# Optimization experiments

Hardware: AMD Instinct MI355X
Metric: run time of the kernel (lower is better)

## Reference

```python
import jax, jax.numpy as jnp
import numpy as np


def setup_inputs() -> dict:
    key = jax.random.key(0)
    ks = jax.random.split(key, 7)
    B, L, D, N = 4, 4096, 1024, 64
    x = jax.random.normal(ks[0], (B, L, D), dtype=jnp.float32)
    # nn.Linear weights: (out_features, in_features)
    W_in = jax.random.normal(ks[1], (N, D), dtype=jnp.float32) * (1.0 / np.sqrt(D))
    W_out = jax.random.normal(ks[2], (D, N), dtype=jnp.float32) * (1.0 / np.sqrt(N))
    log_A = jax.random.normal(ks[3], (N,), dtype=jnp.float32) * 0.02
    B_param = jax.random.normal(ks[4], (N,), dtype=jnp.float32) * 0.02
    C_param = jax.random.normal(ks[5], (N,), dtype=jnp.float32) * 0.02
    log_dt = jnp.float32(np.log(1.0))  # dt_init = 1.0
    return {"x": x, "W_in": W_in, "W_out": W_out, "log_A": log_A,
            "B_param": B_param, "C_param": C_param, "log_dt": log_dt}


def _zoh_discretize(log_A, B_param, log_dt):
    dt = jnp.exp(log_dt)
    A = -jnp.exp(log_A)
    Abar = jnp.exp(A * dt)
    eps = 1e-06
    small = jnp.abs(A) < eps
    denom = jnp.where(small, jnp.ones_like(A), A)
    frac = (Abar - 1.0) / denom
    frac = jnp.where(small, dt, frac)
    Bbar = frac * B_param
    return Abar, Bbar


def reference(x, W_in, W_out, log_A, B_param, C_param, log_dt):
    # x: (B, L, D)
    Bsz, L, D = x.shape
    N = log_A.shape[0]
    Abar, Bbar = _zoh_discretize(log_A, B_param, log_dt)
    u = jnp.einsum('bld,nd->bln', x, W_in)  # (B, L, N)

    def step(h, u_t):
        h = h * Abar + u_t * Bbar  # (B, N)
        return h, h * C_param

    h0 = jnp.zeros((Bsz, N), dtype=x.dtype)
    _, ys = jax.lax.scan(step, h0, jnp.swapaxes(u, 0, 1))  # ys: (L, B, N)
    y = jnp.swapaxes(ys, 0, 1)  # (B, L, N)
    return jnp.einsum('bln,dn->bld', y, W_out)  # (B, L, D)
```

## Files before the change

### kernel.cpp

```cpp
#include <hip/hip_runtime.h>
#include <math.h>

namespace {

constexpr int kB = 4;
constexpr int kL = 4096;
constexpr int kD = 1024;
constexpr int kN = 64;
constexpr int kM = kB * kL;
constexpr size_t kBLN = (size_t)kM * kN;
constexpr int kSplit = 8;
constexpr int kKRange = kD / kSplit;
constexpr int kBK1 = 32;
constexpr int kBK2 = 16;
constexpr int kChunks = 64;
constexpr int kChunkLen = kL / kChunks;
constexpr size_t kHloc = (size_t)kB * kChunks * kN;

template <bool kAtomic>
__global__ __launch_bounds__(64) void k_gemm_in(const float* __restrict__ x,
                                                const float* __restrict__ Win,
                                                float* __restrict__ u) {
  __shared__ __align__(16) float As[kBK1][68];
  __shared__ __align__(16) float Bs[kBK1][68];
  const int t = threadIdx.x;
  const int m_blk = blockIdx.x * 64;
  const int z = blockIdx.y;

  const int tm = t & 7;
  const int tn = t >> 3;
  const int m0 = tm * 8;
  const int n0 = tn * 8;

  const int kk = t & 31;
  const int half = t >> 5;

  float acc[8][8];
#pragma unroll
  for (int i = 0; i < 8; ++i)
#pragma unroll
    for (int j = 0; j < 8; ++j) acc[i][j] = 0.0f;

  for (int kc = 0; kc < kKRange; kc += kBK1) {
    const int k0 = z * kKRange + kc;
#pragma unroll
    for (int i = 0; i < 8; ++i) {
      const int m4 = half * 32 + i * 4;
      const float* src = &x[(size_t)(m_blk + m4) * kD + k0 + kk];
      float4 v = make_float4(src[0], src[kD], src[2 * kD], src[3 * kD]);
      *reinterpret_cast<float4*>(&As[kk][m4]) = v;
    }
#pragma unroll
    for (int i = 0; i < 8; ++i) {
      const int n4 = half * 32 + i * 4;
      const float* src = &Win[(size_t)n4 * kD + k0 + kk];
      float4 v = make_float4(src[0], src[kD], src[2 * kD], src[3 * kD]);
      *reinterpret_cast<float4*>(&Bs[kk][n4]) = v;
    }
    __syncthreads();

#pragma unroll 4
    for (int k = 0; k < kBK1; ++k) {
      float4 a0 = *reinterpret_cast<const float4*>(&As[k][m0]);
      float4 a1 = *reinterpret_cast<const float4*>(&As[k][m0 + 4]);
      float4 b0 = *reinterpret_cast<const float4*>(&Bs[k][n0]);
      float4 b1 = *reinterpret_cast<const float4*>(&Bs[k][n0 + 4]);
      float a[8] = {a0.x, a0.y, a0.z, a0.w, a1.x, a1.y, a1.z, a1.w};
      float b[8] = {b0.x, b0.y, b0.z, b0.w, b1.x, b1.y, b1.z, b1.w};
#pragma unroll
      for (int i = 0; i < 8; ++i)
#pragma unroll
        for (int j = 0; j < 8; ++j) acc[i][j] = fmaf(a[i], b[j], acc[i][j]);
    }
    __syncthreads();
  }

  if constexpr (kAtomic) {
#pragma unroll
    for (int i = 0; i < 8; ++i) {
      float* dst = &u[(size_t)(m_blk + m0 + i) * kN + n0];
#pragma unroll
      for (int j = 0; j < 8; ++j) atomicAdd(dst + j, acc[i][j]);
    }
  } else {
    float* up = u + (size_t)z * kBLN;
#pragma unroll
    for (int i = 0; i < 8; ++i) {
      const size_t o = (size_t)(m_blk + m0 + i) * kN + n0;
      *reinterpret_cast<float4*>(&up[o]) =
          make_float4(acc[i][0], acc[i][1], acc[i][2], acc[i][3]);
      *reinterpret_cast<float4*>(&up[o + 4]) =
          make_float4(acc[i][4], acc[i][5], acc[i][6], acc[i][7]);
    }
  }
}

__device__ __forceinline__ void zoh(const float* __restrict__ logA,
                                    const float* __restrict__ logdt, int n,
                                    float& A, float& dt, float& Abar) {
  dt = expf(logdt[0]);
  A = -expf(logA[n]);
  Abar = expf(A * dt);
}

__device__ __forceinline__ float zoh_bbar(float A, float dt, float Abar,
                                          float Bp) {
  const bool small = fabsf(A) < 1e-6f;
  const float denom = small ? 1.0f : A;
  float frac = (Abar - 1.0f) / denom;
  frac = small ? dt : frac;
  return frac * Bp;
}

template <int kParts>
__global__ __launch_bounds__(64) void k_scan_local(
    const float* __restrict__ logA, const float* __restrict__ Bparam,
    const float* __restrict__ logdt, float* __restrict__ u,
    float* __restrict__ hloc) {
  const int n = threadIdx.x;
  const int c = blockIdx.x;
  const int b = blockIdx.y;
  float A, dt, Abar;
  zoh(logA, logdt, n, A, dt, Abar);
  const float Bbar = zoh_bbar(A, dt, Abar, Bparam[n]);

  const size_t base = ((size_t)b * kL + (size_t)c * kChunkLen) * kN + n;

  float h = 0.0f;
#pragma unroll 8
  for (int s = 0; s < kChunkLen; ++s) {
    const size_t idx = base + (size_t)s * kN;
    float uu = 0.0f;
#pragma unroll
    for (int p = 0; p < kParts; ++p) uu += u[idx + (size_t)p * kBLN];
    const float ub = uu * Bbar;
    h = fmaf(h, Abar, ub);
    u[idx] = ub;
  }
  hloc[((size_t)b * kChunks + c) * kN + n] = h;
}

__global__ __launch_bounds__(64) void k_scan_apply(
    const float* __restrict__ logA, const float* __restrict__ Cparam,
    const float* __restrict__ logdt, const float* __restrict__ u,
    float* __restrict__ ybuf, const float* __restrict__ hloc) {
  const int n = threadIdx.x;
  const int c = blockIdx.x;
  const int b = blockIdx.y;
  float A, dt, Abar;
  zoh(logA, logdt, n, A, dt, Abar);
  const float C = Cparam[n];
  const float AbarC = expf(A * dt * (float)kChunkLen);

  const size_t hbase = (size_t)b * kChunks * kN + n;

  float h = 0.0f;
  if (c > 0) {
    float p0 = hloc[hbase];
    float p1 = (c > 1) ? hloc[hbase + kN] : 0.0f;
    for (int j = 0; j < c; ++j) {
      const float cur = p0;
      p0 = p1;
      p1 = (j + 2 < c) ? hloc[hbase + (size_t)(j + 2) * kN] : 0.0f;
      h = fmaf(h, AbarC, cur);
    }
  }

  const size_t base = ((size_t)b * kL + (size_t)c * kChunkLen) * kN + n;
#pragma unroll 8
  for (int s = 0; s < kChunkLen; ++s) {
    const size_t idx = base + (size_t)s * kN;
    h = fmaf(h, Abar, u[idx]);
    ybuf[idx] = h * C;
  }
}

__global__ __launch_bounds__(128) void k_gemm_out(
    const float* __restrict__ y, const float* __restrict__ Wout,
    float* __restrict__ out) {
  __shared__ __align__(16) float Ys[kBK2][68];
  __shared__ __align__(16) float Ws[kBK2][132];
  const int t = threadIdx.x;
  const int m_blk = blockIdx.x * 64;
  const int d_blk = blockIdx.y * 128;

  const int kk = t & 15;
  const int g = t >> 4;

  const int tm = t & 7;
  const int tn = t >> 3;
  const int m0 = tm * 8;
  const int n0 = tn * 8;

  float acc[8][8];
#pragma unroll
  for (int i = 0; i < 8; ++i)
#pragma unroll
    for (int j = 0; j < 8; ++j) acc[i][j] = 0.0f;

  for (int kc = 0; kc < kN; kc += kBK2) {
#pragma unroll
    for (int i = 0; i < 2; ++i) {
      const int m4 = g * 8 + i * 4;
      const float* src = &y[(size_t)(m_blk + m4) * kN + kc + kk];
      *reinterpret_cast<float4*>(&Ys[kk][m4]) =
          make_float4(src[0], src[kN], src[2 * kN], src[3 * kN]);
    }
#pragma unroll
    for (int i = 0; i < 4; ++i) {
      const int d4 = g * 16 + i * 4;
      const float* src = &Wout[(size_t)(d_blk + d4) * kN + kc + kk];
      *reinterpret_cast<float4*>(&Ws[kk][d4]) =
          make_float4(src[0], src[kN], src[2 * kN], src[3 * kN]);
    }
    __syncthreads();

#pragma unroll 4
    for (int k = 0; k < kBK2; ++k) {
      float4 a0 = *reinterpret_cast<const float4*>(&Ys[k][m0]);
      float4 a1 = *reinterpret_cast<const float4*>(&Ys[k][m0 + 4]);
      float4 b0 = *reinterpret_cast<const float4*>(&Ws[k][n0]);
      float4 b1 = *reinterpret_cast<const float4*>(&Ws[k][n0 + 4]);
      float a[8] = {a0.x, a0.y, a0.z, a0.w, a1.x, a1.y, a1.z, a1.w};
      float b[8] = {b0.x, b0.y, b0.z, b0.w, b1.x, b1.y, b1.z, b1.w};
#pragma unroll
      for (int i = 0; i < 8; ++i)
#pragma unroll
        for (int j = 0; j < 8; ++j) acc[i][j] = fmaf(a[i], b[j], acc[i][j]);
    }
    __syncthreads();
  }

#pragma unroll
  for (int i = 0; i < 8; ++i) {
    const size_t o = (size_t)(m_blk + m0 + i) * kD + d_blk + n0;
    *reinterpret_cast<float4*>(&out[o]) =
        make_float4(acc[i][0], acc[i][1], acc[i][2], acc[i][3]);
    *reinterpret_cast<float4*>(&out[o + 4]) =
        make_float4(acc[i][4], acc[i][5], acc[i][6], acc[i][7]);
  }
}

}

extern "C" void kernel_launch(void* const* d_in, const int* in_sizes, int n_in,
                              void* d_out, int out_size, void* d_ws,
                              size_t ws_size, hipStream_t stream) {
  const float* x = (const float*)d_in[0];
  const float* Win = (const float*)d_in[1];
  const float* Wout = (const float*)d_in[2];
  const float* logA = (const float*)d_in[3];
  const float* Bparam = (const float*)d_in[4];
  const float* Cparam = (const float*)d_in[5];
  const float* logdt = (const float*)d_in[6];
  float* out = (float*)d_out;
  float* ws = (float*)d_ws;

  const bool partials = ws_size >= (8 * kBLN + kHloc) * sizeof(float);

  if (partials) {
    float* hloc = ws + 8 * kBLN;
    k_gemm_in<false><<<dim3(kM / 64, kSplit), 64, 0, stream>>>(x, Win, ws);
    k_scan_local<kSplit><<<dim3(kChunks, kB), 64, 0, stream>>>(
        logA, Bparam, logdt, ws, hloc);
    k_scan_apply<<<dim3(kChunks, kB), 64, 0, stream>>>(
        logA, Cparam, logdt, ws, ws + kBLN, hloc);
    k_gemm_out<<<dim3(kM / 64, kD / 128), 128, 0, stream>>>(ws + kBLN, Wout,
                                                            out);
  } else {
    float* hloc = ws + 2 * kBLN;
    hipMemsetAsync(ws, 0, kBLN * sizeof(float), stream);
    k_gemm_in<true><<<dim3(kM / 64, kSplit), 64, 0, stream>>>(x, Win, ws);
    k_scan_local<1><<<dim3(kChunks, kB), 64, 0, stream>>>(logA, Bparam, logdt,
                                                          ws, hloc);
    k_scan_apply<<<dim3(kChunks, kB), 64, 0, stream>>>(
        logA, Cparam, logdt, ws, ws + kBLN, hloc);
    k_gemm_out<<<dim3(kM / 64, kD / 128), 128, 0, stream>>>(ws + kBLN, Wout,
                                                            out);
  }
}
```

Measured before the change: 206.6 us.

## Prefetch GEMM tiles into registers and split partial-sum reduction into its own kernel

Both GEMM kernels now load the next K-chunk from global memory into registers while the current chunk is computed from shared memory, and they gain a min-blocks-per-SM hint. The reduction of the split-K partials and the Bbar scaling move out of the serial per-chunk scan into a separate fully parallel vectorized kernel. The intent is to hide global load latency and to take the 8-way partial reads off the low-parallelism scan. In exchange there is higher register pressure, one more kernel launch and an extra pass over u. The atomic fallback for small workspaces is removed.

```diff
diff --git a/kernel.cpp b/kernel.cpp
--- a/kernel.cpp
+++ b/kernel.cpp
@@ -17,10 +17,9 @@
 constexpr int kChunkLen = kL / kChunks;
 constexpr size_t kHloc = (size_t)kB * kChunks * kN;
 
-template <bool kAtomic>
-__global__ __launch_bounds__(64) void k_gemm_in(const float* __restrict__ x,
-                                                const float* __restrict__ Win,
-                                                float* __restrict__ u) {
+__global__ __launch_bounds__(64, 2) void k_gemm_in(
+    const float* __restrict__ x, const float* __restrict__ Win,
+    float* __restrict__ u) {
   __shared__ __align__(16) float As[kBK1][68];
   __shared__ __align__(16) float Bs[kBK1][68];
   const int t = threadIdx.x;
@@ -35,29 +34,35 @@
   const int kk = t & 31;
   const int half = t >> 5;
 
+  float4 ra[8], rb[8];
+  auto load_chunk = [&](int kc) {
+    const int k0 = z * kKRange + kc;
+#pragma unroll
+    for (int i = 0; i < 8; ++i) {
+      const int r4 = half * 32 + i * 4;
+      const float* sa = &x[(size_t)(m_blk + r4) * kD + k0 + kk];
+      ra[i] = make_float4(sa[0], sa[kD], sa[2 * kD], sa[3 * kD]);
+      const float* sb = &Win[(size_t)r4 * kD + k0 + kk];
+      rb[i] = make_float4(sb[0], sb[kD], sb[2 * kD], sb[3 * kD]);
+    }
+  };
+
   float acc[8][8];
 #pragma unroll
   for (int i = 0; i < 8; ++i)
 #pragma unroll
     for (int j = 0; j < 8; ++j) acc[i][j] = 0.0f;
 
+  load_chunk(0);
   for (int kc = 0; kc < kKRange; kc += kBK1) {
-    const int k0 = z * kKRange + kc;
 #pragma unroll
     for (int i = 0; i < 8; ++i) {
-      const int m4 = half * 32 + i * 4;
-      const float* src = &x[(size_t)(m_blk + m4) * kD + k0 + kk];
-      float4 v = make_float4(src[0], src[kD], src[2 * kD], src[3 * kD]);
-      *reinterpret_cast<float4*>(&As[kk][m4]) = v;
-    }
-#pragma unroll
-    for (int i = 0; i < 8; ++i) {
-      const int n4 = half * 32 + i * 4;
-      const float* src = &Win[(size_t)n4 * kD + k0 + kk];
-      float4 v = make_float4(src[0], src[kD], src[2 * kD], src[3 * kD]);
-      *reinterpret_cast<float4*>(&Bs[kk][n4]) = v;
-    }
-    __syncthreads();
+      const int r4 = half * 32 + i * 4;
+      *reinterpret_cast<float4*>(&As[kk][r4]) = ra[i];
+      *reinterpret_cast<float4*>(&Bs[kk][r4]) = rb[i];
+    }
+    __syncthreads();
+    if (kc + kBK1 < kKRange) load_chunk(kc + kBK1);
 
 #pragma unroll 4
     for (int k = 0; k < kBK1; ++k) {
@@ -75,23 +80,14 @@
     __syncthreads();
   }
 
-  if constexpr (kAtomic) {
-#pragma unroll
-    for (int i = 0; i < 8; ++i) {
-      float* dst = &u[(size_t)(m_blk + m0 + i) * kN + n0];
-#pragma unroll
-      for (int j = 0; j < 8; ++j) atomicAdd(dst + j, acc[i][j]);
-    }
-  } else {
-    float* up = u + (size_t)z * kBLN;
-#pragma unroll
-    for (int i = 0; i < 8; ++i) {
-      const size_t o = (size_t)(m_blk + m0 + i) * kN + n0;
-      *reinterpret_cast<float4*>(&up[o]) =
-          make_float4(acc[i][0], acc[i][1], acc[i][2], acc[i][3]);
-      *reinterpret_cast<float4*>(&up[o + 4]) =
-          make_float4(acc[i][4], acc[i][5], acc[i][6], acc[i][7]);
-    }
+  float* up = u + (size_t)z * kBLN;
+#pragma unroll
+  for (int i = 0; i < 8; ++i) {
+    const size_t o = (size_t)(m_blk + m0 + i) * kN + n0;
+    *reinterpret_cast<float4*>(&up[o]) =
+        make_float4(acc[i][0], acc[i][1], acc[i][2], acc[i][3]);
+    *reinterpret_cast<float4*>(&up[o + 4]) =
+        make_float4(acc[i][4], acc[i][5], acc[i][6], acc[i][7]);
   }
 }
 
@@ -112,30 +108,50 @@
   return frac * Bp;
 }
 
-template <int kParts>
+__global__ __launch_bounds__(256) void k_reduce(
+    const float* __restrict__ logA, const float* __restrict__ Bparam,
+    const float* __restrict__ logdt, float* __restrict__ u) {
+  __shared__ float sB[kN];
+  const int t = threadIdx.x;
+  if (t < kN) {
+    float A, dt, Abar;
+    zoh(logA, logdt, t, A, dt, Abar);
+    sB[t] = zoh_bbar(A, dt, Abar, Bparam[t]);
+  }
+  __syncthreads();
+
+  const size_t i4 = ((size_t)blockIdx.x * 256 + t) * 4;
+  float4 acc = *reinterpret_cast<const float4*>(&u[i4]);
+#pragma unroll
+  for (int p = 1; p < kSplit; ++p) {
+    float4 v = *reinterpret_cast<const float4*>(&u[i4 + (size_t)p * kBLN]);
+    acc.x += v.x;
+    acc.y += v.y;
+    acc.z += v.z;
+    acc.w += v.w;
+  }
+  const int n0 = (int)(i4 & (kN - 1));
+  acc.x *= sB[n0];
+  acc.y *= sB[n0 + 1];
+  acc.z *= sB[n0 + 2];
+  acc.w *= sB[n0 + 3];
+  *reinterpret_cast<float4*>(&u[i4]) = acc;
+}
+
 __global__ __launch_bounds__(64) void k_scan_local(
-    const float* __restrict__ logA, const float* __restrict__ Bparam,
-    const float* __restrict__ logdt, float* __restrict__ u,
-    float* __restrict__ hloc) {
+    const float* __restrict__ logA, const float* __restrict__ logdt,
+    const float* __restrict__ u, float* __restrict__ hloc) {
   const int n = threadIdx.x;
   const int c = blockIdx.x;
   const int b = blockIdx.y;
   float A, dt, Abar;
   zoh(logA, logdt, n, A, dt, Abar);
-  const float Bbar = zoh_bbar(A, dt, Abar, Bparam[n]);
 
   const size_t base = ((size_t)b * kL + (size_t)c * kChunkLen) * kN + n;
-
   float h = 0.0f;
 #pragma unroll 8
   for (int s = 0; s < kChunkLen; ++s) {
-    const size_t idx = base + (size_t)s * kN;
-    float uu = 0.0f;
-#pragma unroll
-    for (int p = 0; p < kParts; ++p) uu += u[idx + (size_t)p * kBLN];
-    const float ub = uu * Bbar;
-    h = fmaf(h, Abar, ub);
-    u[idx] = ub;
+    h = fmaf(h, Abar, u[base + (size_t)s * kN]);
   }
   hloc[((size_t)b * kChunks + c) * kN + n] = h;
 }
@@ -153,7 +169,6 @@
   const float AbarC = expf(A * dt * (float)kChunkLen);
 
   const size_t hbase = (size_t)b * kChunks * kN + n;
-
   float h = 0.0f;
   if (c > 0) {
     float p0 = hloc[hbase];
@@ -175,7 +190,7 @@
   }
 }
 
-__global__ __launch_bounds__(128) void k_gemm_out(
+__global__ __launch_bounds__(128, 2) void k_gemm_out(
     const float* __restrict__ y, const float* __restrict__ Wout,
     float* __restrict__ out) {
   __shared__ __align__(16) float Ys[kBK2][68];
@@ -192,28 +207,38 @@
   const int m0 = tm * 8;
   const int n0 = tn * 8;
 
-  float acc[8][8];
-#pragma unroll
-  for (int i = 0; i < 8; ++i)
-#pragma unroll
-    for (int j = 0; j < 8; ++j) acc[i][j] = 0.0f;
-
-  for (int kc = 0; kc < kN; kc += kBK2) {
+  float4 ry[2], rw[4];
+  auto load_chunk = [&](int kc) {
 #pragma unroll
     for (int i = 0; i < 2; ++i) {
       const int m4 = g * 8 + i * 4;
-      const float* src = &y[(size_t)(m_blk + m4) * kN + kc + kk];
-      *reinterpret_cast<float4*>(&Ys[kk][m4]) =
-          make_float4(src[0], src[kN], src[2 * kN], src[3 * kN]);
+      const float* s = &y[(size_t)(m_blk + m4) * kN + kc + kk];
+      ry[i] = make_float4(s[0], s[kN], s[2 * kN], s[3 * kN]);
     }
 #pragma unroll
     for (int i = 0; i < 4; ++i) {
       const int d4 = g * 16 + i * 4;
-      const float* src = &Wout[(size_t)(d_blk + d4) * kN + kc + kk];
-      *reinterpret_cast<float4*>(&Ws[kk][d4]) =
-          make_float4(src[0], src[kN], src[2 * kN], src[3 * kN]);
-    }
-    __syncthreads();
+      const float* s = &Wout[(size_t)(d_blk + d4) * kN + kc + kk];
+      rw[i] = make_float4(s[0], s[kN], s[2 * kN], s[3 * kN]);
+    }
+  };
+
+  float acc[8][8];
+#pragma unroll
+  for (int i = 0; i < 8; ++i)
+#pragma unroll
+    for (int j = 0; j < 8; ++j) acc[i][j] = 0.0f;
+
+  load_chunk(0);
+  for (int kc = 0; kc < kN; kc += kBK2) {
+#pragma unroll
+    for (int i = 0; i < 2; ++i)
+      *reinterpret_cast<float4*>(&Ys[kk][g * 8 + i * 4]) = ry[i];
+#pragma unroll
+    for (int i = 0; i < 4; ++i)
+      *reinterpret_cast<float4*>(&Ws[kk][g * 16 + i * 4]) = rw[i];
+    __syncthreads();
+    if (kc + kBK2 < kN) load_chunk(kc + kBK2);
 
 #pragma unroll 4
     for (int k = 0; k < kBK2; ++k) {
@@ -255,27 +280,14 @@
   const float* logdt = (const float*)d_in[6];
   float* out = (float*)d_out;
   float* ws = (float*)d_ws;
-
-  const bool partials = ws_size >= (8 * kBLN + kHloc) * sizeof(float);
-
-  if (partials) {
-    float* hloc = ws + 8 * kBLN;
-    k_gemm_in<false><<<dim3(kM / 64, kSplit), 64, 0, stream>>>(x, Win, ws);
-    k_scan_local<kSplit><<<dim3(kChunks, kB), 64, 0, stream>>>(
-        logA, Bparam, logdt, ws, hloc);
-    k_scan_apply<<<dim3(kChunks, kB), 64, 0, stream>>>(
-        logA, Cparam, logdt, ws, ws + kBLN, hloc);
-    k_gemm_out<<<dim3(kM / 64, kD / 128), 128, 0, stream>>>(ws + kBLN, Wout,
-                                                            out);
-  } else {
-    float* hloc = ws + 2 * kBLN;
-    hipMemsetAsync(ws, 0, kBLN * sizeof(float), stream);
-    k_gemm_in<true><<<dim3(kM / 64, kSplit), 64, 0, stream>>>(x, Win, ws);
-    k_scan_local<1><<<dim3(kChunks, kB), 64, 0, stream>>>(logA, Bparam, logdt,
-                                                          ws, hloc);
-    k_scan_apply<<<dim3(kChunks, kB), 64, 0, stream>>>(
-        logA, Cparam, logdt, ws, ws + kBLN, hloc);
-    k_gemm_out<<<dim3(kM / 64, kD / 128), 128, 0, stream>>>(ws + kBLN, Wout,
-                                                            out);
-  }
-}
+  float* hloc = ws + 8 * kBLN;
+
+  k_gemm_in<<<dim3(kM / 64, kSplit), 64, 0, stream>>>(x, Win, ws);
+  k_reduce<<<dim3((int)(kBLN / 1024)), 256, 0, stream>>>(logA, Bparam, logdt,
+                                                         ws);
+  k_scan_local<<<dim3(kChunks, kB), 64, 0, stream>>>(logA, logdt, ws, hloc);
+  k_scan_apply<<<dim3(kChunks, kB), 64, 0, stream>>>(logA, Cparam, logdt, ws,
+                                                     ws + kBLN, hloc);
+  k_gemm_out<<<dim3(kM / 64, kD / 128), 128, 0, stream>>>(ws + kBLN, Wout,
+                                                          out);
+}
```

Result: faster. 202.3 us (-2.1%).
